# Kernel optimization log

Hardware: AMD Instinct MI355X
Metric: run time of the kernel (lower is better)

The kernel has to match this reference:

```python
import jax, jax.numpy as jnp
import numpy as np

B, N, D_V, D_H, D_K = 1024, 131072, 256, 256, 256


def setup_inputs() -> dict:
    key = jax.random.key(0)
    ks = jax.random.split(key, 12)
    s = 0.02
    V = jax.random.normal(ks[0], (B, D_V), dtype=jnp.float32)
    H = jax.random.normal(ks[1], (N, D_H), dtype=jnp.float32)
    batch_idx = jnp.sort(jax.random.randint(ks[2], (N,), 0, B)).astype(jnp.int32)
    Wq = jax.random.normal(ks[3], (D_K, D_V), dtype=jnp.float32) / np.sqrt(D_V)
    bq = jnp.zeros((D_K,), dtype=jnp.float32)
    Wk = jax.random.normal(ks[4], (D_K, D_H), dtype=jnp.float32) / np.sqrt(D_H)
    bk = jnp.zeros((D_K,), dtype=jnp.float32)
    Wv = jax.random.normal(ks[5], (D_V, D_H), dtype=jnp.float32) / np.sqrt(D_H)
    bv = jnp.zeros((D_V,), dtype=jnp.float32)
    Wo = jax.random.normal(ks[6], (D_V, 2 * D_V), dtype=jnp.float32) / np.sqrt(2 * D_V)
    bo = jnp.zeros((D_V,), dtype=jnp.float32)
    return {"V": V, "H": H, "batch_idx": batch_idx,
            "Wq": Wq, "bq": bq, "Wk": Wk, "bk": bk,
            "Wv": Wv, "bv": bv, "Wo": Wo, "bo": bo}


def reference(V, H, batch_idx, Wq, bq, Wk, bk, Wv, bv, Wo, bo):
    nb = V.shape[0]
    Q = V @ Wq.T + bq            # [B, d_k] one query per graph
    K = H @ Wk.T + bk            # [N, d_k]
    Vval = H @ Wv.T + bv         # [N, d_v]
    scale = 1.0 / jnp.sqrt(jnp.asarray(K.shape[-1], K.dtype))
    # ragged attention scores: each node attends to its graph's query
    scores = jnp.einsum('nd,nd->n', K, Q[batch_idx]) * scale   # [N]
    m = jax.ops.segment_max(scores, batch_idx, num_segments=nb)  # [B]
    e = jnp.exp(scores - m[batch_idx])
    denom = jax.ops.segment_sum(e, batch_idx, num_segments=nb)   # [B]
    attn = e / denom[batch_idx]                                  # [N]
    H_tilde = jax.ops.segment_sum(attn[:, None] * Vval, batch_idx, num_segments=nb)  # [B, d_v]
    U = jnp.concatenate([V, H_tilde], axis=-1)                   # [B, 2*d_v]
    out = U @ Wo.T + bo                                          # [B, d_v]
    # graphs with zero nodes pass V through unchanged
    count = jax.ops.segment_sum(jnp.ones_like(scores), batch_idx, num_segments=nb)
    return jnp.where((count > 0)[:, None], out, V)
```

## Files before the change

### kernel.cpp

```cpp
#include <hip/hip_runtime.h>
#include <math.h>

#define D 256
#define TWOD 512
#define BB 1024
#define NN 131072
#define LOG2E 1.4426950408889634f

typedef float v4f __attribute__((ext_vector_type(4)));

__device__ __forceinline__ v4f ldg_nt(const float* p, bool valid) {
  v4f z = {0.f, 0.f, 0.f, 0.f};
  if (valid) z = __builtin_nontemporal_load((const v4f*)p);
  return z;
}

__device__ __forceinline__ float dot4(v4f a, v4f b) {
  return fmaf(a.w, b.w, fmaf(a.z, b.z, fmaf(a.y, b.y, a.x * b.x)));
}

__device__ __forceinline__ float pack4(float d0, float d1, float d2, float d3) {
  float a01 = d0 + __shfl_xor(d1, 4);
  float a23 = d2 + __shfl_xor(d3, 4);
  float s = a01 + __shfl_xor(a23, 8);
  s += __shfl_xor(s, 1);
  s += __shfl_xor(s, 2);
  s += __shfl_xor(s, 16);
  s += __shfl_xor(s, 32);
  return s;
}

__global__ __launch_bounds__(256) void t_kernel(
    const float* __restrict__ Wv, const float* __restrict__ Wo,
    const int* __restrict__ bidx,
    float* __restrict__ WvT, float* __restrict__ WoT,
    int* __restrict__ offs) {
  const int blk = blockIdx.x;
  const int t = threadIdx.x;
  if (blk < 48) {
    __shared__ float tile[64][65];
    const float* src; float* dst; int r0, c0, C;
    if (blk < 16) { src = Wv; dst = WvT; C = 256; r0 = (blk >> 2) * 64; c0 = (blk & 3) * 64; }
    else          { int b = blk - 16; src = Wo; dst = WoT; C = 512; r0 = (b >> 3) * 64; c0 = (b & 7) * 64; }
    const int lane = t & 63, sr = t >> 6;
    #pragma unroll 4
    for (int rr = 0; rr < 16; ++rr) {
      const int r = rr * 4 + sr;
      tile[r][lane] = src[(size_t)(r0 + r) * C + c0 + lane];
    }
    __syncthreads();
    #pragma unroll 4
    for (int rr = 0; rr < 16; ++rr) {
      const int r = rr * 4 + sr;
      dst[(size_t)(c0 + r) * 256 + r0 + lane] = tile[lane][r];
    }
  } else {
    const int i = (blk - 48) * 256 + t;
    if (i >= NN) return;
    const int b1 = bidx[i];
    const int b2 = (i + 1 < NN) ? bidx[i + 1] : BB;
    if (i == 0) {
      for (int b = 0; b <= b1; ++b) offs[b] = 0;
    }
    for (int b = b1 + 1; b <= b2; ++b) offs[b] = i + 1;
  }
}

__global__ __launch_bounds__(1024) void f_kernel(
    const float* __restrict__ H, const float* __restrict__ V,
    const float* __restrict__ Wq, const float* __restrict__ Wk,
    const float* __restrict__ bq, const int* __restrict__ offs,
    const float* __restrict__ WvT, const float* __restrict__ WoT,
    const float* __restrict__ bv, const float* __restrict__ bo,
    float* __restrict__ out) {
  __shared__ __align__(16) char smem[61440];
  float* partq = (float*)smem;
  float (*ss)[D] = (float(*)[D])smem;
  float* Vs   = (float*)(smem + 16384);
  float* sN2  = (float*)(smem + 16384);
  float* q1s4 = (float*)(smem + 20480);
  float* Us2  = (float*)(smem + 20480);
  float (*part)[4][D] = (float(*)[4][D])(smem + 28672);
  __shared__ float sm[16], sd[16];

  const int t = threadIdx.x;
  const int wave = t >> 6, lane = t & 63;
  const int blk = blockIdx.x;
  const int b0 = blk * 4;

  {
    const int i = t >> 8, d = t & 255;
    Vs[i * 256 + d] = V[(size_t)(b0 + i) * D + d];
  }
  __syncthreads();

  {
    const int rot = (lane >> 2) & 3;
    const v4f vb0 = *(const v4f*)&Vs[0 * 256 + lane * 4];
    const v4f vb1 = *(const v4f*)&Vs[1 * 256 + lane * 4];
    const v4f vb2 = *(const v4f*)&Vs[2 * 256 + lane * 4];
    const v4f vb3 = *(const v4f*)&Vs[3 * 256 + lane * 4];
    #pragma unroll
    for (int ii = 0; ii < 4; ++ii) {
      const int cb = wave * 16 + ii * 4;
      const v4f r0 = *(const v4f*)(Wq + (size_t)(cb + (rot ^ 0)) * D + lane * 4);
      const v4f r1 = *(const v4f*)(Wq + (size_t)(cb + (rot ^ 1)) * D + lane * 4);
      const v4f r2 = *(const v4f*)(Wq + (size_t)(cb + (rot ^ 2)) * D + lane * 4);
      const v4f r3 = *(const v4f*)(Wq + (size_t)(cb + (rot ^ 3)) * D + lane * 4);
      const float s0 = pack4(dot4(r0, vb0), dot4(r1, vb0), dot4(r2, vb0), dot4(r3, vb0));
      const float s1 = pack4(dot4(r0, vb1), dot4(r1, vb1), dot4(r2, vb1), dot4(r3, vb1));
      const float s2 = pack4(dot4(r0, vb2), dot4(r1, vb2), dot4(r2, vb2), dot4(r3, vb2));
      const float s3 = pack4(dot4(r0, vb3), dot4(r1, vb3), dot4(r2, vb3), dot4(r3, vb3));
      if (lane < 16 && (lane & 3) == 0) {
        v4f o = {s0, s1, s2, s3};
        *(v4f*)&q1s4[(cb + rot) * 4] = o;
      }
    }
  }
  __syncthreads();

  {
    const int i = wave & 3, kq = wave >> 2;
    v4f aq = {0.f, 0.f, 0.f, 0.f};
    const int kb = kq * 64;
    for (int kk = 0; kk < 64; ++kk) {
      const int k = kb + kk;
      const v4f w4 = *(const v4f*)(Wk + (size_t)k * D + lane * 4);
      aq += w4 * (q1s4[k * 4 + i] + bq[k]);
    }
    *(v4f*)&partq[(kq * 4 + i) * 256 + lane * 4] = aq;
  }
  __syncthreads();

  const int ib = wave >> 2, qq = wave & 3;
  const int bb = b0 + ib;
  const int start = offs[bb], end = offs[bb + 1];

  v4f q4;
  {
    const v4f p0 = *(const v4f*)&partq[(0 * 4 + ib) * 256 + lane * 4];
    const v4f p1 = *(const v4f*)&partq[(1 * 4 + ib) * 256 + lane * 4];
    const v4f p2 = *(const v4f*)&partq[(2 * 4 + ib) * 256 + lane * 4];
    const v4f p3 = *(const v4f*)&partq[(3 * 4 + ib) * 256 + lane * 4];
    q4 = (p0 + p1) + (p2 + p3);
  }
  __syncthreads();

  float m = -1e30f, den = 0.f;
  v4f acc = {0.f, 0.f, 0.f, 0.f};
  {
    const float SC = 0.0625f * LOG2E;
    const int odd = lane & 1;
    int n = start + qq * 2;
    v4f c0 = ldg_nt(H + (size_t)n * D + lane * 4, n < end);
    v4f c1 = ldg_nt(H + (size_t)(n + 1) * D + lane * 4, n + 1 < end);
    while (n < end) {
      const int nn = n + 8;
      v4f p0 = ldg_nt(H + (size_t)nn * D + lane * 4, nn < end);
      v4f p1 = ldg_nt(H + (size_t)(nn + 1) * D + lane * 4, nn + 1 < end);

      const float d0 = dot4(c0, q4);
      const float d1 = dot4(c1, q4);
      const float mine = odd ? d1 : d0;
      const float oth  = odd ? d0 : d1;
      float s = mine + __shfl_xor(oth, 1);
      s += __shfl_xor(s, 2);
      s += __shfl_xor(s, 4);
      s += __shfl_xor(s, 8);
      s += __shfl_xor(s, 16);
      s += __shfl_xor(s, 32);
      const float sc = (n + odd < end) ? s * SC : -1e30f;

      const float mm = fmaxf(sc, __shfl_xor(sc, 1));
      const float nm = fmaxf(m, mm);
      const float f = exp2f(m - nm);
      const float w = exp2f(sc - nm);
      const float wx = __shfl_xor(w, 1);
      const float wr0 = odd ? wx : w;
      const float wr1 = odd ? w : wx;
      den = fmaf(den, f, w + wx);
      acc = acc * f + c0 * wr0 + c1 * wr1;
      m = nm;

      c0 = p0; c1 = p1; n = nn;
    }
  }
  *(v4f*)&ss[wave][lane * 4] = acc;
  if (lane == 0) { sm[wave] = m; sd[wave] = den; }
  __syncthreads();

  {
    const int i = t >> 8, d = t & 255;
    const int w0 = i * 4;
    const float m0 = sm[w0], m1 = sm[w0 + 1], m2 = sm[w0 + 2], m3 = sm[w0 + 3];
    const float M = fmaxf(fmaxf(m0, m1), fmaxf(m2, m3));
    const float f0 = exp2f(m0 - M), f1 = exp2f(m1 - M);
    const float f2 = exp2f(m2 - M), f3 = exp2f(m3 - M);
    const float Dn = sd[w0] * f0 + sd[w0 + 1] * f1 + sd[w0 + 2] * f2 + sd[w0 + 3] * f3;
    const float inv = (Dn > 0.f) ? (1.f / Dn) : 0.f;
    const float sv = (ss[w0][d] * f0 + ss[w0 + 1][d] * f1 +
                      ss[w0 + 2][d] * f2 + ss[w0 + 3][d] * f3) * inv;
    const float vv = V[(size_t)(b0 + i) * D + d];
    __syncthreads();
    sN2[d * 4 + i] = sv;
    Us2[d * 4 + i] = vv;
  }
  __syncthreads();

  v4f a0 = {0.f, 0.f, 0.f, 0.f}, a1 = a0, a2 = a0, a3 = a0;
  {
    const int hb = wave * 16;
    #pragma unroll 4
    for (int hh = 0; hh < 16; ++hh) {
      const int h = hb + hh;
      const v4f w4 = *(const v4f*)(WvT + (size_t)h * D + lane * 4);
      const v4f s4 = *(const v4f*)&sN2[h * 4];
      a0 += w4 * s4.x; a1 += w4 * s4.y; a2 += w4 * s4.z; a3 += w4 * s4.w;
    }
  }
  if (wave >= 8) {
    *(v4f*)&part[wave - 8][0][lane * 4] = a0;
    *(v4f*)&part[wave - 8][1][lane * 4] = a1;
    *(v4f*)&part[wave - 8][2][lane * 4] = a2;
    *(v4f*)&part[wave - 8][3][lane * 4] = a3;
  }
  __syncthreads();
  if (wave < 8) {
    v4f p0 = *(const v4f*)&part[wave][0][lane * 4];
    v4f p1 = *(const v4f*)&part[wave][1][lane * 4];
    v4f p2 = *(const v4f*)&part[wave][2][lane * 4];
    v4f p3 = *(const v4f*)&part[wave][3][lane * 4];
    *(v4f*)&part[wave][0][lane * 4] = a0 + p0;
    *(v4f*)&part[wave][1][lane * 4] = a1 + p1;
    *(v4f*)&part[wave][2][lane * 4] = a2 + p2;
    *(v4f*)&part[wave][3][lane * 4] = a3 + p3;
  }
  __syncthreads();
  {
    const int i = t >> 8, d = t & 255;
    float s = bv[d];
    #pragma unroll
    for (int w = 0; w < 8; ++w) s += part[w][i][d];
    Us2[(D + d) * 4 + i] = s;
  }
  __syncthreads();

  a0 = (v4f){0.f, 0.f, 0.f, 0.f}; a1 = a0; a2 = a0; a3 = a0;
  {
    const int kb = wave * 32;
    #pragma unroll 4
    for (int kk = 0; kk < 32; ++kk) {
      const int k = kb + kk;
      const v4f w4 = *(const v4f*)(WoT + (size_t)k * D + lane * 4);
      const v4f u4 = *(const v4f*)&Us2[k * 4];
      a0 += w4 * u4.x; a1 += w4 * u4.y; a2 += w4 * u4.z; a3 += w4 * u4.w;
    }
  }
  if (wave >= 8) {
    *(v4f*)&part[wave - 8][0][lane * 4] = a0;
    *(v4f*)&part[wave - 8][1][lane * 4] = a1;
    *(v4f*)&part[wave - 8][2][lane * 4] = a2;
    *(v4f*)&part[wave - 8][3][lane * 4] = a3;
  }
  __syncthreads();
  if (wave < 8) {
    v4f p0 = *(const v4f*)&part[wave][0][lane * 4];
    v4f p1 = *(const v4f*)&part[wave][1][lane * 4];
    v4f p2 = *(const v4f*)&part[wave][2][lane * 4];
    v4f p3 = *(const v4f*)&part[wave][3][lane * 4];
    *(v4f*)&part[wave][0][lane * 4] = a0 + p0;
    *(v4f*)&part[wave][1][lane * 4] = a1 + p1;
    *(v4f*)&part[wave][2][lane * 4] = a2 + p2;
    *(v4f*)&part[wave][3][lane * 4] = a3 + p3;
  }
  __syncthreads();
  {
    const int i = t >> 8, d = t & 255;
    const int bb2 = b0 + i;
    float s = bo[d];
    #pragma unroll
    for (int w = 0; w < 8; ++w) s += part[w][i][d];
    const int c = offs[bb2 + 1] - offs[bb2];
    out[(size_t)bb2 * D + d] = (c > 0) ? s : Us2[d * 4 + i];
  }
}

extern "C" void kernel_launch(void* const* d_in, const int* in_sizes, int n_in,
                              void* d_out, int out_size, void* d_ws, size_t ws_size,
                              hipStream_t stream) {
  const float* V   = (const float*)d_in[0];
  const float* H   = (const float*)d_in[1];
  const int* bidx  = (const int*)d_in[2];
  const float* Wq  = (const float*)d_in[3];
  const float* bq  = (const float*)d_in[4];
  const float* Wk  = (const float*)d_in[5];
  const float* Wv  = (const float*)d_in[7];
  const float* bv  = (const float*)d_in[8];
  const float* Wo  = (const float*)d_in[9];
  const float* bo  = (const float*)d_in[10];
  float* out = (float*)d_out;

  float* ws  = (float*)d_ws;
  float* WvT = ws;
  float* WoT = WvT + D * D;
  int* offs  = (int*)(WoT + TWOD * D);

  hipLaunchKernelGGL(t_kernel, dim3(560), dim3(256), 0, stream,
                     Wv, Wo, bidx, WvT, WoT, offs);
  hipLaunchKernelGGL(f_kernel, dim3(BB / 4), dim3(1024), 0, stream,
                     H, V, Wq, Wk, bq, offs, WvT, WoT, bv, bo, out);
}
```

Before: 56.65 us.

## Fold Wq·Wk and Wo·Wv weight products into a prep kernel

A prep kernel now precomputes the fused query-key matrix (Wq^T Wk), the fused output-value matrix (Wo_right·Wv), and the folded biases. The main kernel then computes q with a single 256x256 matvec per graph instead of two chained projections, and applies one 512-wide output GEMV instead of a separate Wv projection followed by Wo. This removes a dependent matvec stage and a reduction/sync round per block. In exchange the prep kernel does two 256^3 weight GEMMs with naive per-thread loops, and floating-point summation order changes.

Measured after the change: 46.25 us. 18.4% less time.

```diff
diff --git a/kernel.cpp b/kernel.cpp
--- a/kernel.cpp
+++ b/kernel.cpp
@@ -19,43 +19,74 @@
   return fmaf(a.w, b.w, fmaf(a.z, b.z, fmaf(a.y, b.y, a.x * b.x)));
 }
 
-__device__ __forceinline__ float pack4(float d0, float d1, float d2, float d3) {
-  float a01 = d0 + __shfl_xor(d1, 4);
-  float a23 = d2 + __shfl_xor(d3, 4);
-  float s = a01 + __shfl_xor(a23, 8);
-  s += __shfl_xor(s, 1);
-  s += __shfl_xor(s, 2);
-  s += __shfl_xor(s, 16);
-  s += __shfl_xor(s, 32);
-  return s;
-}
-
-__global__ __launch_bounds__(256) void t_kernel(
-    const float* __restrict__ Wv, const float* __restrict__ Wo,
-    const int* __restrict__ bidx,
-    float* __restrict__ WvT, float* __restrict__ WoT,
+__global__ __launch_bounds__(256) void prep_kernel(
+    const float* __restrict__ Wq, const float* __restrict__ bq,
+    const float* __restrict__ Wk, const float* __restrict__ Wv,
+    const float* __restrict__ bv, const float* __restrict__ Wo,
+    const float* __restrict__ bo, const int* __restrict__ bidx,
+    float* __restrict__ Mt, float* __restrict__ WfT,
+    float* __restrict__ bqt, float* __restrict__ cvec,
     int* __restrict__ offs) {
   const int blk = blockIdx.x;
   const int t = threadIdx.x;
-  if (blk < 48) {
+  if (blk < 64) {
+    const int d0 = blk * 4;
+    float a0 = 0.f, a1 = 0.f, a2 = 0.f, a3 = 0.f;
+    for (int e = 0; e < D; ++e) {
+      const float wk = Wk[(size_t)e * D + t];
+      const float* wqr = Wq + (size_t)e * D + d0;
+      a0 = fmaf(wqr[0], wk, a0);
+      a1 = fmaf(wqr[1], wk, a1);
+      a2 = fmaf(wqr[2], wk, a2);
+      a3 = fmaf(wqr[3], wk, a3);
+    }
+    Mt[(size_t)(d0 + 0) * D + t] = a0;
+    Mt[(size_t)(d0 + 1) * D + t] = a1;
+    Mt[(size_t)(d0 + 2) * D + t] = a2;
+    Mt[(size_t)(d0 + 3) * D + t] = a3;
+  } else if (blk < 128) {
+    const int h0 = (blk - 64) * 4;
+    float a0 = 0.f, a1 = 0.f, a2 = 0.f, a3 = 0.f;
+    for (int v = 0; v < D; ++v) {
+      const float wo = Wo[(size_t)t * TWOD + D + v];
+      const float* wvr = Wv + (size_t)v * D + h0;
+      a0 = fmaf(wvr[0], wo, a0);
+      a1 = fmaf(wvr[1], wo, a1);
+      a2 = fmaf(wvr[2], wo, a2);
+      a3 = fmaf(wvr[3], wo, a3);
+    }
+    WfT[(size_t)(D + h0 + 0) * D + t] = a0;
+    WfT[(size_t)(D + h0 + 1) * D + t] = a1;
+    WfT[(size_t)(D + h0 + 2) * D + t] = a2;
+    WfT[(size_t)(D + h0 + 3) * D + t] = a3;
+  } else if (blk < 144) {
     __shared__ float tile[64][65];
-    const float* src; float* dst; int r0, c0, C;
-    if (blk < 16) { src = Wv; dst = WvT; C = 256; r0 = (blk >> 2) * 64; c0 = (blk & 3) * 64; }
-    else          { int b = blk - 16; src = Wo; dst = WoT; C = 512; r0 = (b >> 3) * 64; c0 = (b & 7) * 64; }
+    const int b = blk - 128;
+    const int r0 = (b >> 2) * 64, c0 = (b & 3) * 64;
     const int lane = t & 63, sr = t >> 6;
     #pragma unroll 4
     for (int rr = 0; rr < 16; ++rr) {
       const int r = rr * 4 + sr;
-      tile[r][lane] = src[(size_t)(r0 + r) * C + c0 + lane];
+      tile[r][lane] = Wo[(size_t)(r0 + r) * TWOD + c0 + lane];
     }
     __syncthreads();
     #pragma unroll 4
     for (int rr = 0; rr < 16; ++rr) {
       const int r = rr * 4 + sr;
-      dst[(size_t)(c0 + r) * 256 + r0 + lane] = tile[lane][r];
-    }
+      WfT[(size_t)(c0 + r) * D + r0 + lane] = tile[lane][r];
+    }
+  } else if (blk == 144) {
+    float a = 0.f;
+    for (int e = 0; e < D; ++e)
+      a = fmaf(Wk[(size_t)e * D + t], bq[e], a);
+    bqt[t] = a;
+  } else if (blk == 145) {
+    float a = bo[t];
+    for (int v = 0; v < D; ++v)
+      a = fmaf(Wo[(size_t)t * TWOD + D + v], bv[v], a);
+    cvec[t] = a;
   } else {
-    const int i = (blk - 48) * 256 + t;
+    const int i = (blk - 146) * 256 + t;
     if (i >= NN) return;
     const int b1 = bidx[i];
     const int b2 = (i + 1 < NN) ? bidx[i + 1] : BB;
@@ -68,19 +99,15 @@
 
 __global__ __launch_bounds__(1024) void f_kernel(
     const float* __restrict__ H, const float* __restrict__ V,
-    const float* __restrict__ Wq, const float* __restrict__ Wk,
-    const float* __restrict__ bq, const int* __restrict__ offs,
-    const float* __restrict__ WvT, const float* __restrict__ WoT,
-    const float* __restrict__ bv, const float* __restrict__ bo,
-    float* __restrict__ out) {
-  __shared__ __align__(16) char smem[61440];
-  float* partq = (float*)smem;
+    const float* __restrict__ Mt, const float* __restrict__ bqt,
+    const int* __restrict__ offs, const float* __restrict__ WfT,
+    const float* __restrict__ cvec, float* __restrict__ out) {
+  __shared__ __align__(16) char smem[32768 + 4096 + 8192];
+  float (*partq)[4][D] = (float(*)[4][D])smem;
   float (*ss)[D] = (float(*)[D])smem;
-  float* Vs   = (float*)(smem + 16384);
-  float* sN2  = (float*)(smem + 16384);
-  float* q1s4 = (float*)(smem + 20480);
-  float* Us2  = (float*)(smem + 20480);
-  float (*part)[4][D] = (float(*)[4][D])(smem + 28672);
+  float (*part)[4][D] = (float(*)[4][D])smem;
+  float* Vs  = (float*)(smem + 32768);
+  float* Us2 = (float*)(smem + 36864);
   __shared__ float sm[16], sd[16];
 
   const int t = threadIdx.x;
@@ -95,40 +122,34 @@
   __syncthreads();
 
   {
-    const int rot = (lane >> 2) & 3;
-    const v4f vb0 = *(const v4f*)&Vs[0 * 256 + lane * 4];
-    const v4f vb1 = *(const v4f*)&Vs[1 * 256 + lane * 4];
-    const v4f vb2 = *(const v4f*)&Vs[2 * 256 + lane * 4];
-    const v4f vb3 = *(const v4f*)&Vs[3 * 256 + lane * 4];
-    #pragma unroll
-    for (int ii = 0; ii < 4; ++ii) {
-      const int cb = wave * 16 + ii * 4;
-      const v4f r0 = *(const v4f*)(Wq + (size_t)(cb + (rot ^ 0)) * D + lane * 4);
-      const v4f r1 = *(const v4f*)(Wq + (size_t)(cb + (rot ^ 1)) * D + lane * 4);
-      const v4f r2 = *(const v4f*)(Wq + (size_t)(cb + (rot ^ 2)) * D + lane * 4);
-      const v4f r3 = *(const v4f*)(Wq + (size_t)(cb + (rot ^ 3)) * D + lane * 4);
-      const float s0 = pack4(dot4(r0, vb0), dot4(r1, vb0), dot4(r2, vb0), dot4(r3, vb0));
-      const float s1 = pack4(dot4(r0, vb1), dot4(r1, vb1), dot4(r2, vb1), dot4(r3, vb1));
-      const float s2 = pack4(dot4(r0, vb2), dot4(r1, vb2), dot4(r2, vb2), dot4(r3, vb2));
-      const float s3 = pack4(dot4(r0, vb3), dot4(r1, vb3), dot4(r2, vb3), dot4(r3, vb3));
-      if (lane < 16 && (lane & 3) == 0) {
-        v4f o = {s0, s1, s2, s3};
-        *(v4f*)&q1s4[(cb + rot) * 4] = o;
-      }
-    }
-  }
-  __syncthreads();
-
-  {
-    const int i = wave & 3, kq = wave >> 2;
-    v4f aq = {0.f, 0.f, 0.f, 0.f};
-    const int kb = kq * 64;
-    for (int kk = 0; kk < 64; ++kk) {
-      const int k = kb + kk;
-      const v4f w4 = *(const v4f*)(Wk + (size_t)k * D + lane * 4);
-      aq += w4 * (q1s4[k * 4 + i] + bq[k]);
-    }
-    *(v4f*)&partq[(kq * 4 + i) * 256 + lane * 4] = aq;
+    v4f a0 = {0.f, 0.f, 0.f, 0.f}, a1 = a0, a2 = a0, a3 = a0;
+    const int db = wave * 16;
+    #pragma unroll 4
+    for (int dd = 0; dd < 16; ++dd) {
+      const int d = db + dd;
+      const v4f w4 = *(const v4f*)(Mt + (size_t)d * D + lane * 4);
+      a0 += w4 * Vs[0 * 256 + d];
+      a1 += w4 * Vs[1 * 256 + d];
+      a2 += w4 * Vs[2 * 256 + d];
+      a3 += w4 * Vs[3 * 256 + d];
+    }
+    if (wave >= 8) {
+      *(v4f*)&partq[wave - 8][0][lane * 4] = a0;
+      *(v4f*)&partq[wave - 8][1][lane * 4] = a1;
+      *(v4f*)&partq[wave - 8][2][lane * 4] = a2;
+      *(v4f*)&partq[wave - 8][3][lane * 4] = a3;
+    }
+    __syncthreads();
+    if (wave < 8) {
+      v4f p0 = *(const v4f*)&partq[wave][0][lane * 4];
+      v4f p1 = *(const v4f*)&partq[wave][1][lane * 4];
+      v4f p2 = *(const v4f*)&partq[wave][2][lane * 4];
+      v4f p3 = *(const v4f*)&partq[wave][3][lane * 4];
+      *(v4f*)&partq[wave][0][lane * 4] = a0 + p0;
+      *(v4f*)&partq[wave][1][lane * 4] = a1 + p1;
+      *(v4f*)&partq[wave][2][lane * 4] = a2 + p2;
+      *(v4f*)&partq[wave][3][lane * 4] = a3 + p3;
+    }
   }
   __syncthreads();
 
@@ -136,14 +157,9 @@
   const int bb = b0 + ib;
   const int start = offs[bb], end = offs[bb + 1];
 
-  v4f q4;
-  {
-    const v4f p0 = *(const v4f*)&partq[(0 * 4 + ib) * 256 + lane * 4];
-    const v4f p1 = *(const v4f*)&partq[(1 * 4 + ib) * 256 + lane * 4];
-    const v4f p2 = *(const v4f*)&partq[(2 * 4 + ib) * 256 + lane * 4];
-    const v4f p3 = *(const v4f*)&partq[(3 * 4 + ib) * 256 + lane * 4];
-    q4 = (p0 + p1) + (p2 + p3);
-  }
+  v4f q4 = *(const v4f*)(bqt + lane * 4);
+  #pragma unroll
+  for (int w = 0; w < 8; ++w) q4 += *(const v4f*)&partq[w][ib][lane * 4];
   __syncthreads();
 
   float m = -1e30f, den = 0.f;
@@ -200,84 +216,44 @@
     const float inv = (Dn > 0.f) ? (1.f / Dn) : 0.f;
     const float sv = (ss[w0][d] * f0 + ss[w0 + 1][d] * f1 +
                       ss[w0 + 2][d] * f2 + ss[w0 + 3][d] * f3) * inv;
-    const float vv = V[(size_t)(b0 + i) * D + d];
-    __syncthreads();
-    sN2[d * 4 + i] = sv;
-    Us2[d * 4 + i] = vv;
-  }
-  __syncthreads();
-
-  v4f a0 = {0.f, 0.f, 0.f, 0.f}, a1 = a0, a2 = a0, a3 = a0;
-  {
-    const int hb = wave * 16;
-    #pragma unroll 4
-    for (int hh = 0; hh < 16; ++hh) {
-      const int h = hb + hh;
-      const v4f w4 = *(const v4f*)(WvT + (size_t)h * D + lane * 4);
-      const v4f s4 = *(const v4f*)&sN2[h * 4];
-      a0 += w4 * s4.x; a1 += w4 * s4.y; a2 += w4 * s4.z; a3 += w4 * s4.w;
-    }
-  }
-  if (wave >= 8) {
-    *(v4f*)&part[wave - 8][0][lane * 4] = a0;
-    *(v4f*)&part[wave - 8][1][lane * 4] = a1;
-    *(v4f*)&part[wave - 8][2][lane * 4] = a2;
-    *(v4f*)&part[wave - 8][3][lane * 4] = a3;
-  }
-  __syncthreads();
-  if (wave < 8) {
-    v4f p0 = *(const v4f*)&part[wave][0][lane * 4];
-    v4f p1 = *(const v4f*)&part[wave][1][lane * 4];
-    v4f p2 = *(const v4f*)&part[wave][2][lane * 4];
-    v4f p3 = *(const v4f*)&part[wave][3][lane * 4];
-    *(v4f*)&part[wave][0][lane * 4] = a0 + p0;
-    *(v4f*)&part[wave][1][lane * 4] = a1 + p1;
-    *(v4f*)&part[wave][2][lane * 4] = a2 + p2;
-    *(v4f*)&part[wave][3][lane * 4] = a3 + p3;
-  }
-  __syncthreads();
-  {
-    const int i = t >> 8, d = t & 255;
-    float s = bv[d];
-    #pragma unroll
-    for (int w = 0; w < 8; ++w) s += part[w][i][d];
-    Us2[(D + d) * 4 + i] = s;
-  }
-  __syncthreads();
-
-  a0 = (v4f){0.f, 0.f, 0.f, 0.f}; a1 = a0; a2 = a0; a3 = a0;
-  {
+    Us2[d * 4 + i] = Vs[i * 256 + d];
+    Us2[(D + d) * 4 + i] = sv;
+  }
+  __syncthreads();
+
+  {
+    v4f a0 = {0.f, 0.f, 0.f, 0.f}, a1 = a0, a2 = a0, a3 = a0;
     const int kb = wave * 32;
     #pragma unroll 4
     for (int kk = 0; kk < 32; ++kk) {
       const int k = kb + kk;
-      const v4f w4 = *(const v4f*)(WoT + (size_t)k * D + lane * 4);
+      const v4f w4 = *(const v4f*)(WfT + (size_t)k * D + lane * 4);
       const v4f u4 = *(const v4f*)&Us2[k * 4];
       a0 += w4 * u4.x; a1 += w4 * u4.y; a2 += w4 * u4.z; a3 += w4 * u4.w;
     }
-  }
-  if (wave >= 8) {
-    *(v4f*)&part[wave - 8][0][lane * 4] = a0;
-    *(v4f*)&part[wave - 8][1][lane * 4] = a1;
-    *(v4f*)&part[wave - 8][2][lane * 4] = a2;
-    *(v4f*)&part[wave - 8][3][lane * 4] = a3;
-  }
-  __syncthreads();
-  if (wave < 8) {
-    v4f p0 = *(const v4f*)&part[wave][0][lane * 4];
-    v4f p1 = *(const v4f*)&part[wave][1][lane * 4];
-    v4f p2 = *(const v4f*)&part[wave][2][lane * 4];
-    v4f p3 = *(const v4f*)&part[wave][3][lane * 4];
-    *(v4f*)&part[wave][0][lane * 4] = a0 + p0;
-    *(v4f*)&part[wave][1][lane * 4] = a1 + p1;
-    *(v4f*)&part[wave][2][lane * 4] = a2 + p2;
-    *(v4f*)&part[wave][3][lane * 4] = a3 + p3;
+    if (wave >= 8) {
+      *(v4f*)&part[wave - 8][0][lane * 4] = a0;
+      *(v4f*)&part[wave - 8][1][lane * 4] = a1;
+      *(v4f*)&part[wave - 8][2][lane * 4] = a2;
+      *(v4f*)&part[wave - 8][3][lane * 4] = a3;
+    }
+    __syncthreads();
+    if (wave < 8) {
+      v4f p0 = *(const v4f*)&part[wave][0][lane * 4];
+      v4f p1 = *(const v4f*)&part[wave][1][lane * 4];
+      v4f p2 = *(const v4f*)&part[wave][2][lane * 4];
+      v4f p3 = *(const v4f*)&part[wave][3][lane * 4];
+      *(v4f*)&part[wave][0][lane * 4] = a0 + p0;
+      *(v4f*)&part[wave][1][lane * 4] = a1 + p1;
+      *(v4f*)&part[wave][2][lane * 4] = a2 + p2;
+      *(v4f*)&part[wave][3][lane * 4] = a3 + p3;
+    }
   }
   __syncthreads();
   {
     const int i = t >> 8, d = t & 255;
     const int bb2 = b0 + i;
-    float s = bo[d];
+    float s = cvec[d];
     #pragma unroll
     for (int w = 0; w < 8; ++w) s += part[w][i][d];
     const int c = offs[bb2 + 1] - offs[bb2];
@@ -301,12 +277,15 @@
   float* out = (float*)d_out;
 
   float* ws  = (float*)d_ws;
-  float* WvT = ws;
-  float* WoT = WvT + D * D;
-  int* offs  = (int*)(WoT + TWOD * D);
-
-  hipLaunchKernelGGL(t_kernel, dim3(560), dim3(256), 0, stream,
-                     Wv, Wo, bidx, WvT, WoT, offs);
+  float* Mt  = ws;
+  float* WfT = Mt + D * D;
+  float* bqt = WfT + TWOD * D;
+  float* cv  = bqt + D;
+  int* offs  = (int*)(cv + D);
+
+  hipLaunchKernelGGL(prep_kernel, dim3(658), dim3(256), 0, stream,
+                     Wq, bq, Wk, Wv, bv, Wo, bo, bidx,
+                     Mt, WfT, bqt, cv, offs);
   hipLaunchKernelGGL(f_kernel, dim3(BB / 4), dim3(1024), 0, stream,
-                     H, V, Wq, Wk, bq, offs, WvT, WoT, bv, bo, out);
-}
+                     H, V, Mt, bqt, offs, WfT, cv, out);
+}
```
